# Performance work log

Measured on AMD Instinct MI355X. Metric: run time of the kernel, lower is better.

## Reference

```python
import jax, jax.numpy as jnp
import numpy as np

KERNEL = 7
DS_LIM = 0.01
ALPHA_M = 1.0


def _smooth_field(field):
    # field [3,D,H,W] -> depthwise mean filter with kernel 7, SAME padding
    k = KERNEL
    w = jnp.ones((3, 1, k, k, k), dtype=field.dtype) / (k ** 3)
    out = jax.lax.conv_general_dilated(
        field[None], w, (1, 1, 1), 'SAME',
        dimension_numbers=('NCDHW', 'OIDHW', 'NCDHW'),
        feature_group_count=3)
    return out[0]


def _trilinear(vol, coords):
    # vol [B,D,H,W]; coords [B,3,D,H,W] in voxel units
    B, D, H, W = vol.shape
    cz = jnp.clip(coords[:, 0], 0.0, D - 1.0)
    cy = jnp.clip(coords[:, 1], 0.0, H - 1.0)
    cx = jnp.clip(coords[:, 2], 0.0, W - 1.0)
    z0 = jnp.floor(cz).astype(jnp.int32); z1 = jnp.minimum(z0 + 1, D - 1)
    y0 = jnp.floor(cy).astype(jnp.int32); y1 = jnp.minimum(y0 + 1, H - 1)
    x0 = jnp.floor(cx).astype(jnp.int32); x1 = jnp.minimum(x0 + 1, W - 1)
    fz = cz - z0; fy = cy - y0; fx = cx - x0
    b = jnp.arange(B)[:, None, None, None]
    g = lambda zi, yi, xi: vol[b, zi, yi, xi]
    c00 = g(z0, y0, x0) * (1 - fx) + g(z0, y0, x1) * fx
    c01 = g(z0, y1, x0) * (1 - fx) + g(z0, y1, x1) * fx
    c10 = g(z1, y0, x0) * (1 - fx) + g(z1, y0, x1) * fx
    c11 = g(z1, y1, x0) * (1 - fx) + g(z1, y1, x1) * fx
    c0 = c00 * (1 - fy) + c01 * fy
    c1 = c10 * (1 - fy) + c11 * fy
    return c0 * (1 - fz) + c1 * fz


def setup_inputs() -> dict:
    key = jax.random.key(0)
    ks = jax.random.split(key, 8)
    B, C, L = 8, 128, 5
    D = H = W = 96
    return {
        'encode_ds': jax.random.normal(ks[0], (B, C, L, L, L), jnp.float32),
        'orig': jax.random.normal(ks[1], (B, 1, D, H, W), jnp.float32),
        'mask': jax.random.uniform(ks[2], (B, 1, D, H, W), jnp.float32),
        'c1_w': jax.random.normal(ks[3], (1, C, 1, 1, 1), jnp.float32) * 0.05,
        'c1_b': jnp.zeros((1,), jnp.float32),
        'f1_w': jax.random.normal(ks[4], (1, L ** 3), jnp.float32) * 0.1,
        'f1_b': jnp.zeros((1,), jnp.float32),
        'offset_field': jax.random.normal(ks[5], (3, D, H, W), jnp.float32),
    }


def reference(encode_ds, orig, mask, c1_w, c1_b, f1_w, f1_b, offset_field):
    B = encode_ds.shape[0]
    # 1x1x1 Conv3d (128 -> 1) is a per-voxel channel contraction
    a = jnp.einsum('bcdhw,c->bdhw', encode_ds, c1_w[0, :, 0, 0, 0]) + c1_b[0]
    a = a.reshape(B, -1)                                   # [B, 125]
    alpha = jax.nn.sigmoid(a @ f1_w[0] + f1_b[0]) * ALPHA_M  # [B]

    # deform: smoothed, ds_lim-clamped offset field scaled by per-sample alpha
    field = jnp.clip(_smooth_field(offset_field), -DS_LIM, DS_LIM)  # [3,D,H,W]
    _, _, D, H, W = orig.shape
    base = jnp.stack(jnp.meshgrid(jnp.arange(D, dtype=orig.dtype),
                                  jnp.arange(H, dtype=orig.dtype),
                                  jnp.arange(W, dtype=orig.dtype),
                                  indexing='ij'))          # [3,D,H,W]
    scale = jnp.array([D, H, W], orig.dtype).reshape(1, 3, 1, 1, 1)
    disp = alpha[:, None, None, None, None] * field[None] * scale  # [B,3,D,H,W]
    coords = base[None] + disp

    def_ = _trilinear(orig[:, 0], coords)[:, None]
    mask_d = _trilinear(mask[:, 0], coords)[:, None]
    return def_, mask_d
```

## Files before the change

### kernel.cpp

```cpp
#include <hip/hip_runtime.h>
#include <hip/hip_fp16.h>
#include <math.h>

#define DD 96
#define VOX (96*96*96)
#define NB 8
#define NC 128
#define L3 125

#define BTS 16
#define BNT 6
#define BNTILE (BNT*BNT*BNT)
#define BHZ 22
#define BHY 22
#define XSN (BHY * 23 * BTS)

#define TZ 12
#define TY 8
#define TX 32
#define NTZ 8
#define NTY 12
#define NTX 3
#define STILE (NTZ*NTY*NTX)
#define HZS 14
#define HYS 10
#define HXS 34
#define HXP 35
#define HN (HZS*HYS*HXS)
#define HLDS (HZS*HYS*HXP)

typedef float vfloat2 __attribute__((ext_vector_type(2)));
typedef float vfloat4 __attribute__((ext_vector_type(4)));

static __device__ __forceinline__ vfloat2 h2f(__half2 h) {
    float2 t = __half22float2(h);
    vfloat2 r; r.x = t.x; r.y = t.y;
    return r;
}

__global__ __launch_bounds__(256) void blur_alpha(
        const float* __restrict__ in, float* __restrict__ out,
        const float* __restrict__ enc,
        const float* __restrict__ c1_w, const float* __restrict__ c1_b,
        const float* __restrict__ f1_w, const float* __restrict__ f1_b,
        float* __restrict__ alpha) {
    __shared__ float xs[XSN];
    __shared__ float red[4];
    int tid = threadIdx.x;

    if (blockIdx.x >= 3 * BNTILE) {
        int b = blockIdx.x - 3 * BNTILE;
        const float4* e4 = (const float4*)(enc + (size_t)b * NC * L3);
        float s = 0.f;
        for (int j = tid; j < (NC * L3) / 4; j += 256) {
            float4 v = e4[j];
            int f = j * 4;
            s += v.x * c1_w[(f + 0) / L3] * f1_w[(f + 0) % L3];
            s += v.y * c1_w[(f + 1) / L3] * f1_w[(f + 1) % L3];
            s += v.z * c1_w[(f + 2) / L3] * f1_w[(f + 2) % L3];
            s += v.w * c1_w[(f + 3) / L3] * f1_w[(f + 3) % L3];
        }
        for (int off = 32; off > 0; off >>= 1) s += __shfl_down(s, off, 64);
        int lane = tid & 63, wid = tid >> 6;
        if (lane == 0) red[wid] = s;
        __syncthreads();
        if (tid == 0) {
            float tot = red[0] + red[1] + red[2] + red[3];
            float fwsum = 0.f;
            for (int v = 0; v < L3; ++v) fwsum += f1_w[v];
            float x = tot + c1_b[0] * fwsum + f1_b[0];
            alpha[b] = 1.f / (1.f + expf(-x));
        }
        return;
    }

    int blk = blockIdx.x;
    int c = blk / BNTILE;
    int t = blk % BNTILE;
    int tz = t / (BNT * BNT), ty = (t / BNT) % BNT, tx = t % BNT;
    int bz = tz * BTS, by = ty * BTS, bx = tx * BTS;
    const float* ib = in + (size_t)c * VOX;

    for (int rr = tid; rr < BHY * BHZ; rr += 256) {
        int hy = rr / BHZ, hz = rr - (rr / BHZ) * BHZ;
        int gz = bz + hz - 3, gy = by + hy - 3;
        float* xrow = &xs[(hy * 23 + hz) * 16];
        if ((unsigned)gz >= DD || (unsigned)gy >= DD) {
            #pragma unroll
            for (int xo = 0; xo < 16; ++xo) xrow[xo] = 0.f;
            continue;
        }
        const float* rp = ib + (gz * DD + gy) * DD;
        int base = bx - 4;
        if (base < 0) base = 0;
        if (base > DD - 28) base = DD - 28;
        const float4* p4 = (const float4*)(rp + base);
        float w[28];
        #pragma unroll
        for (int q = 0; q < 7; ++q) {
            float4 t4 = p4[q];
            w[q * 4 + 0] = t4.x; w[q * 4 + 1] = t4.y;
            w[q * 4 + 2] = t4.z; w[q * 4 + 3] = t4.w;
        }
        float v[22];
        if (bx == 0) {
            v[0] = v[1] = v[2] = 0.f;
            #pragma unroll
            for (int j = 3; j < 22; ++j) v[j] = w[j - 3];
        } else if (bx == DD - BTS) {
            #pragma unroll
            for (int j = 0; j < 19; ++j) v[j] = w[j + 9];
            v[19] = v[20] = v[21] = 0.f;
        } else {
            #pragma unroll
            for (int j = 0; j < 22; ++j) v[j] = w[j + 1];
        }
        float s = v[0] + v[1] + v[2] + v[3] + v[4] + v[5] + v[6];
        xrow[0] = s;
        #pragma unroll
        for (int xo = 1; xo < 16; ++xo) {
            s += v[xo + 6] - v[xo - 1];
            xrow[xo] = s;
        }
    }
    __syncthreads();

    for (int cc = tid; cc < BHZ * BTS; cc += 256) {
        int hz = cc >> 4, xo = cc & 15;
        int base = hz * 16 + xo;
        float s = 0.f;
        #pragma unroll
        for (int hy = 0; hy < 7; ++hy) s += xs[hy * 368 + base];
        #pragma unroll
        for (int yo = 0; yo < 16; ++yo) {
            float old = xs[yo * 368 + base];
            float nxt = (yo < 15) ? xs[(yo + 7) * 368 + base] : 0.f;
            xs[yo * 368 + base] = s;
            s += nxt - old;
        }
    }
    __syncthreads();

    {
        int yo = tid >> 4, xo = tid & 15;
        int base = yo * 368 + xo;
        float s = 0.f;
        #pragma unroll
        for (int hz = 0; hz < 7; ++hz) s += xs[base + hz * 16];
        float* ob = out + (size_t)c * VOX + (by + yo) * DD + bx + xo;
        #pragma unroll
        for (int zo = 0; zo < 16; ++zo) {
            float v = s * (1.0f / 343.0f);
            v = fminf(fmaxf(v, -0.01f), 0.01f) * 96.0f;
            ob[(size_t)(bz + zo) * DD * DD] = v;
            s += xs[base + (zo + 7) * 16] - xs[base + zo * 16];
        }
    }
}

__global__ __launch_bounds__(256, 8) void sample_tile(
        const float* __restrict__ orig,
        const float* __restrict__ mask,
        const float* __restrict__ field,
        const float* __restrict__ alpha,
        float* __restrict__ out) {
    __shared__ __half2 tile[HLDS];

    int blk = blockIdx.x;
    int b = blk / STILE;
    int r = blk % STILE;
    int o = r & 7;
    int l = r >> 3;
    int zh = o >> 2;
    int yq = o & 3;
    int lz4 = l / 9, ly3 = (l / 3) % 3, lx3 = l % 3;
    int tz = zh * 4 + lz4;
    int ty = yq * 3 + ly3;
    int tx = lx3;
    int bz = tz * TZ, by = ty * TY, bx = tx * TX;

    const float* ob = orig + (size_t)b * VOX;
    const float* mb = mask + (size_t)b * VOX;
    int tid = threadIdx.x;

    for (int i = tid; i < HN; i += 256) {
        int hz = i / (HYS * HXS);
        int rr = i - hz * (HYS * HXS);
        int hy = rr / HXS;
        int hx = rr - hy * HXS;
        int gz = min(max(bz + hz - 1, 0), DD - 1);
        int gy = min(max(by + hy - 1, 0), DD - 1);
        int gx = min(max(bx + hx - 1, 0), DD - 1);
        int g = (gz * DD + gy) * DD + gx;
        tile[(hz * HYS + hy) * HXP + hx] = __floats2half2_rn(ob[g], mb[g]);
    }
    float a = alpha[b];
    __syncthreads();

    const vfloat4* fz4 = (const vfloat4*)field;
    const vfloat4* fy4 = (const vfloat4*)(field + VOX);
    const vfloat4* fx4 = (const vfloat4*)(field + 2 * VOX);
    vfloat4* oD = (vfloat4*)(out);
    vfloat4* oM = (vfloat4*)(out + (size_t)NB * VOX);

    int lz  = tid >> 6;
    int ly  = (tid >> 3) & 7;
    int lxq = tid & 7;
    int gy  = by + ly;
    int gx0 = bx + 4 * lxq;
    float gyf = (float)gy;
    float gx0f = (float)gx0;
    float c1z = (float)(1 - bz), c1y = (float)(1 - by), c1x = (float)(1 - bx);

    auto samp = [&](float gzf, float dzv, float dyv, float dxv,
                    float gxf) -> vfloat2 {
        float cz = fminf(fmaxf(fmaf(a, dzv, gzf), 0.f), (float)(DD - 1)) + c1z;
        float cy = fminf(fmaxf(fmaf(a, dyv, gyf), 0.f), (float)(DD - 1)) + c1y;
        float cx = fminf(fmaxf(fmaf(a, dxv, gxf), 0.f), (float)(DD - 1)) + c1x;
        float flz = floorf(cz), fly = floorf(cy), flx = floorf(cx);
        float fzf = cz - flz, fyf = cy - fly, fxf = cx - flx;
        int iz = (int)flz, iy = (int)fly, ix = (int)flx;

        const __half2* tp = tile + (iz * HYS + iy) * HXP + ix;
        vfloat2 v000 = h2f(tp[0]);
        vfloat2 v001 = h2f(tp[1]);
        vfloat2 v010 = h2f(tp[HXP]);
        vfloat2 v011 = h2f(tp[HXP + 1]);
        vfloat2 v100 = h2f(tp[HYS * HXP]);
        vfloat2 v101 = h2f(tp[HYS * HXP + 1]);
        vfloat2 v110 = h2f(tp[(HYS + 1) * HXP]);
        vfloat2 v111 = h2f(tp[(HYS + 1) * HXP + 1]);

        vfloat2 FX = {fxf, fxf}, FY = {fyf, fyf}, FZ = {fzf, fzf};
        vfloat2 c00 = v000 + FX * (v001 - v000);
        vfloat2 c01 = v010 + FX * (v011 - v010);
        vfloat2 c10 = v100 + FX * (v101 - v100);
        vfloat2 c11 = v110 + FX * (v111 - v110);
        vfloat2 c0 = c00 + FY * (c01 - c00);
        vfloat2 c1 = c10 + FY * (c11 - c10);
        return c0 + FZ * (c1 - c0);
    };

    int vp4 = (((bz + lz) * DD + gy) * DD + gx0) >> 2;
    vfloat4 dz = fz4[vp4], dy = fy4[vp4], dx = fx4[vp4];
    size_t ob0 = (size_t)b * (VOX / 4);

    #pragma unroll
    for (int it = 0; it < TZ / 4; ++it) {
        vfloat4 dzn = {0,0,0,0}, dyn = {0,0,0,0}, dxn = {0,0,0,0};
        if (it < TZ / 4 - 1) {
            int vq = vp4 + DD * DD;
            dzn = fz4[vq]; dyn = fy4[vq]; dxn = fx4[vq];
        }
        float gzf = (float)(bz + 4 * it + lz);

        vfloat2 r0 = samp(gzf, dz.x, dy.x, dx.x, gx0f);
        vfloat2 r1 = samp(gzf, dz.y, dy.y, dx.y, gx0f + 1.f);
        vfloat2 r2 = samp(gzf, dz.z, dy.z, dx.z, gx0f + 2.f);
        vfloat2 r3 = samp(gzf, dz.w, dy.w, dx.w, gx0f + 3.f);

        vfloat4 vD = {r0.x, r1.x, r2.x, r3.x};
        vfloat4 vM = {r0.y, r1.y, r2.y, r3.y};
        __builtin_nontemporal_store(vD, &oD[ob0 + vp4]);
        __builtin_nontemporal_store(vM, &oM[ob0 + vp4]);

        vp4 += DD * DD;
        dz = dzn; dy = dyn; dx = dxn;
    }
}

extern "C" void kernel_launch(void* const* d_in, const int* in_sizes, int n_in,
                              void* d_out, int out_size, void* d_ws, size_t ws_size,
                              hipStream_t stream) {
    const float* enc   = (const float*)d_in[0];
    const float* orig  = (const float*)d_in[1];
    const float* mask  = (const float*)d_in[2];
    const float* c1_w  = (const float*)d_in[3];
    const float* c1_b  = (const float*)d_in[4];
    const float* f1_w  = (const float*)d_in[5];
    const float* f1_b  = (const float*)d_in[6];
    const float* offs  = (const float*)d_in[7];
    float* out = (float*)d_out;

    float* ws = (float*)d_ws;
    float* alpha = ws;
    float* fieldB = ws + 16;

    blur_alpha<<<3 * BNTILE + NB, 256, 0, stream>>>(
        offs, fieldB, enc, c1_w, c1_b, f1_w, f1_b, alpha);
    sample_tile<<<NB * STILE, 256, 0, stream>>>(orig, mask, fieldB, alpha, out);
}
```

Before: 169.4 us.

## Halve z-extent of smoothing tiles and pad shared row stride

The box-filter smoothing kernel now uses 16x16x8 output tiles instead of 16x16x16, doubling the number of blocks. The shared x-partial buffer is smaller, so the y-pass fits in a single iteration of 256 threads. The row stride is padded to 225 to reduce LDS bank conflicts. More blocks improve parallelism and occupancy, at the cost of more redundant z-halo loads (14 rows loaded per 8 outputs instead of 22 per 16).

Measured after the change: 163.9 us. 1.03x faster.

```diff
diff --git a/kernel.cpp b/kernel.cpp
--- a/kernel.cpp
+++ b/kernel.cpp
@@ -8,12 +8,16 @@
 #define NC 128
 #define L3 125
 
+#define BTZ 8
 #define BTS 16
-#define BNT 6
-#define BNTILE (BNT*BNT*BNT)
-#define BHZ 22
+#define NBZ 12
+#define NBY 6
+#define NBX 6
+#define BNTILE (NBZ*NBY*NBX)
+#define BHZ 14
 #define BHY 22
-#define XSN (BHY * 23 * BTS)
+#define XROW 225
+#define XSN (BHY * XROW)
 
 #define TZ 12
 #define TY 8
@@ -77,14 +81,14 @@
     int blk = blockIdx.x;
     int c = blk / BNTILE;
     int t = blk % BNTILE;
-    int tz = t / (BNT * BNT), ty = (t / BNT) % BNT, tx = t % BNT;
-    int bz = tz * BTS, by = ty * BTS, bx = tx * BTS;
+    int tz = t / (NBY * NBX), ty = (t / NBX) % NBY, tx = t % NBX;
+    int bz = tz * BTZ, by = ty * BTS, bx = tx * BTS;
     const float* ib = in + (size_t)c * VOX;
 
     for (int rr = tid; rr < BHY * BHZ; rr += 256) {
         int hy = rr / BHZ, hz = rr - (rr / BHZ) * BHZ;
         int gz = bz + hz - 3, gy = by + hy - 3;
-        float* xrow = &xs[(hy * 23 + hz) * 16];
+        float* xrow = &xs[hy * XROW + hz * 16];
         if ((unsigned)gz >= DD || (unsigned)gy >= DD) {
             #pragma unroll
             for (int xo = 0; xo < 16; ++xo) xrow[xo] = 0.f;
@@ -125,17 +129,17 @@
     }
     __syncthreads();
 
-    for (int cc = tid; cc < BHZ * BTS; cc += 256) {
-        int hz = cc >> 4, xo = cc & 15;
+    if (tid < BHZ * BTS) {
+        int hz = tid >> 4, xo = tid & 15;
         int base = hz * 16 + xo;
         float s = 0.f;
         #pragma unroll
-        for (int hy = 0; hy < 7; ++hy) s += xs[hy * 368 + base];
+        for (int hy = 0; hy < 7; ++hy) s += xs[hy * XROW + base];
         #pragma unroll
         for (int yo = 0; yo < 16; ++yo) {
-            float old = xs[yo * 368 + base];
-            float nxt = (yo < 15) ? xs[(yo + 7) * 368 + base] : 0.f;
-            xs[yo * 368 + base] = s;
+            float old = xs[yo * XROW + base];
+            float nxt = (yo < 15) ? xs[(yo + 7) * XROW + base] : 0.f;
+            xs[yo * XROW + base] = s;
             s += nxt - old;
         }
     }
@@ -143,13 +147,13 @@
 
     {
         int yo = tid >> 4, xo = tid & 15;
-        int base = yo * 368 + xo;
+        int base = yo * XROW + xo;
         float s = 0.f;
         #pragma unroll
         for (int hz = 0; hz < 7; ++hz) s += xs[base + hz * 16];
         float* ob = out + (size_t)c * VOX + (by + yo) * DD + bx + xo;
         #pragma unroll
-        for (int zo = 0; zo < 16; ++zo) {
+        for (int zo = 0; zo < BTZ; ++zo) {
             float v = s * (1.0f / 343.0f);
             v = fminf(fmaxf(v, -0.01f), 0.01f) * 96.0f;
             ob[(size_t)(bz + zo) * DD * DD] = v;
```
